# Optimization experiments

Measured on AMD Instinct MI355X. Metric: run time of the kernel, lower is better.

The kernel has to match this reference:

```python
import jax, jax.numpy as jnp
import numpy as np

D_MODEL = 1024
HEAD_SIZE = 64

def setup_inputs() -> dict:
    key = jax.random.key(0)
    ks = jax.random.split(key, 7)
    s = 1.0 / np.sqrt(D_MODEL)
    x = jax.random.normal(ks[0], (4, 4096, D_MODEL), dtype=jnp.float32)
    Wq = jax.random.uniform(ks[1], (D_MODEL, HEAD_SIZE), jnp.float32, -s, s)
    bq = jax.random.uniform(ks[2], (HEAD_SIZE,), jnp.float32, -s, s)
    Wk = jax.random.uniform(ks[3], (D_MODEL, HEAD_SIZE), jnp.float32, -s, s)
    bk = jax.random.uniform(ks[4], (HEAD_SIZE,), jnp.float32, -s, s)
    Wv = jax.random.uniform(ks[5], (D_MODEL, HEAD_SIZE), jnp.float32, -s, s)
    bv = jax.random.uniform(ks[6], (HEAD_SIZE,), jnp.float32, -s, s)
    return {"x": x, "Wq": Wq, "bq": bq, "Wk": Wk, "bk": bk, "Wv": Wv, "bv": bv}

def reference(x, Wq, bq, Wk, bk, Wv, bv):
    # x: [B, S, D]; projections to [B, S, H]
    Q = jnp.einsum('bsd,dh->bsh', x, Wq) + bq
    K = jnp.einsum('bsd,dh->bsh', x, Wk) + bk
    V = jnp.einsum('bsd,dh->bsh', x, Wv) + bv
    scores = jnp.einsum('bqh,bkh->bqk', Q, K) / jnp.sqrt(jnp.float32(HEAD_SIZE))
    attn = jax.nn.softmax(scores, axis=-1)  # [B, S, S]
    return jnp.einsum('bqk,bkh->bqh', attn, V)
```

## Files before the change

kernel.cpp:

```cpp
#include <hip/hip_runtime.h>
#include <hip/hip_bf16.h>


#define S_LEN 4096
#define D_MODEL 1024

typedef __attribute__((ext_vector_type(8))) short bf16x8;
typedef __attribute__((ext_vector_type(4))) float f32x4;
typedef __attribute__((ext_vector_type(16))) float f32x16;

__device__ inline short f2bf(float f) {
    union { float f; unsigned u; } v;
    v.f = f;
    unsigned r = v.u + 0x7fffu + ((v.u >> 16) & 1u);
    return (short)(r >> 16);
}

__device__ inline unsigned cvt_pk(float lo, float hi) {
    unsigned r;
    asm("v_cvt_pk_bf16_f32 %0, %1, %2" : "=v"(r) : "v"(lo), "v"(hi));
    return r;
}

__device__ inline void pl32swap(unsigned& a, unsigned& b) {
    asm("v_permlane32_swap_b32 %0, %1" : "+v"(a), "+v"(b));
}

__device__ inline f32x16 fzero16() {
    f32x16 z;
#pragma unroll
    for (int i = 0; i < 16; ++i) z[i] = 0.f;
    return z;
}

__device__ inline void gload_lds16(const void* g, void* l) {
    __builtin_amdgcn_global_load_lds((const __attribute__((address_space(1))) void*)g,
                                     (__attribute__((address_space(3))) void*)l, 16, 0, 0);
}

__global__ void prep_w(const float* __restrict__ Wq, const float* __restrict__ Wk,
                       const float* __restrict__ Wv, short* __restrict__ WtF) {
    int idx = blockIdx.x * 256 + threadIdx.x;
    int j = idx & 7;
    int lane = (idx >> 3) & 63;
    int f = idx >> 9;
    int ntg = f % 12;
    int kb = f / 12;
    int k = (kb >> 1) * 64 + (kb & 1) * 32 + (lane >> 4) * 8 + j;
    int c = ntg * 16 + (lane & 15);
    const float* W = (c < 64) ? Wq : (c < 128 ? Wk : Wv);
    WtF[idx] = f2bf(W[k * 64 + (c & 63)]);
}

__launch_bounds__(256)
__global__ void proj_kernel(const float* __restrict__ x, const short* __restrict__ WtF,
                            const float* __restrict__ bq, const float* __restrict__ bk,
                            const float* __restrict__ bv,
                            short* __restrict__ Qb, short* __restrict__ Kb,
                            short* __restrict__ Vt) {
    __shared__ short vsm[64][40];
    const float CEXP = 0.18033688011112042f;
    int w = threadIdx.x >> 6;
    int lane = threadIdx.x & 63;
    int g = lane >> 4, ln = lane & 15;
    int rt = w >> 1, nh = w & 1;
    int rowbase = blockIdx.x * 32;

    f32x4 acc[6];
#pragma unroll
    for (int i = 0; i < 6; ++i) acc[i] = (f32x4){0.f, 0.f, 0.f, 0.f};

    const float* xw = x + (size_t)(rowbase + rt * 16 + ln) * D_MODEL + g * 8;

    auto loadF = [&](bf16x8* F, int t) {
#pragma unroll
        for (int kk = 0; kk < 2; ++kk)
#pragma unroll
            for (int nt = 0; nt < 6; ++nt)
                F[kk * 6 + nt] = *(const bf16x8*)(WtF
                    + ((((t * 2 + kk) * 12 + nh * 6 + nt) << 9) + lane * 8));
    };

    auto computeF = [&](const bf16x8* F, const f32x4& X0, const f32x4& X1,
                        const f32x4& X2, const f32x4& X3) {
        union { bf16x8 v; unsigned u[4]; } A;
        A.u[0] = cvt_pk(X0[0], X0[1]);
        A.u[1] = cvt_pk(X0[2], X0[3]);
        A.u[2] = cvt_pk(X1[0], X1[1]);
        A.u[3] = cvt_pk(X1[2], X1[3]);
#pragma unroll
        for (int nt = 0; nt < 6; ++nt)
            acc[nt] = __builtin_amdgcn_mfma_f32_16x16x32_bf16(A.v, F[nt], acc[nt], 0, 0, 0);
        A.u[0] = cvt_pk(X2[0], X2[1]);
        A.u[1] = cvt_pk(X2[2], X2[3]);
        A.u[2] = cvt_pk(X3[0], X3[1]);
        A.u[3] = cvt_pk(X3[2], X3[3]);
#pragma unroll
        for (int nt = 0; nt < 6; ++nt)
            acc[nt] = __builtin_amdgcn_mfma_f32_16x16x32_bf16(A.v, F[6 + nt], acc[nt], 0, 0, 0);
    };

    bf16x8 Fa[12], Fb[12];
    loadF(Fa, 0);
    f32x4 XA0 = *(const f32x4*)(xw);
    f32x4 XA1 = *(const f32x4*)(xw + 4);
    f32x4 XA2 = *(const f32x4*)(xw + 32);
    f32x4 XA3 = *(const f32x4*)(xw + 36);
    f32x4 XB0 = *(const f32x4*)(xw + 64);
    f32x4 XB1 = *(const f32x4*)(xw + 68);
    f32x4 XB2 = *(const f32x4*)(xw + 96);
    f32x4 XB3 = *(const f32x4*)(xw + 100);

#pragma unroll 1
    for (int t = 0; t < 16; t += 2) {
        loadF(Fb, t + 1 > 15 ? 15 : t + 1);
        computeF(Fa, XA0, XA1, XA2, XA3);
        {
            int nx = t + 2 > 15 ? 15 : t + 2;
            const float* xn = xw + nx * 64;
            XA0 = *(const f32x4*)(xn);
            XA1 = *(const f32x4*)(xn + 4);
            XA2 = *(const f32x4*)(xn + 32);
            XA3 = *(const f32x4*)(xn + 36);
        }
        loadF(Fa, t + 2 > 15 ? 15 : t + 2);
        computeF(Fb, XB0, XB1, XB2, XB3);
        {
            int nx = t + 3 > 15 ? 15 : t + 3;
            const float* xn = xw + nx * 64;
            XB0 = *(const f32x4*)(xn);
            XB1 = *(const f32x4*)(xn + 4);
            XB2 = *(const f32x4*)(xn + 32);
            XB3 = *(const f32x4*)(xn + 36);
        }
    }

#pragma unroll
    for (int nt = 0; nt < 6; ++nt) {
        int c = nh * 96 + nt * 16 + ln;
        int proj = c >> 6;
        int h = c & 63;
        float bias = (proj == 0 ? bq : (proj == 1 ? bk : bv))[h];
#pragma unroll
        for (int r = 0; r < 4; ++r) {
            int srow = rowbase + rt * 16 + g * 4 + r;
            float v = acc[nt][r] + bias;
            if (proj == 0) v *= CEXP;
            short hv = f2bf(v);
            if (proj == 0) {
                Qb[(size_t)srow * 64 + h] = hv;
            } else if (proj == 1) {
                Kb[(size_t)srow * 64 + h] = hv;
            } else {
                vsm[h][rt * 16 + g * 4 + r] = hv;
            }
        }
    }
    __syncthreads();
    {
        int t = threadIdx.x;
        int h = t >> 2, c = t & 3;
        bf16x8 val = *(const bf16x8*)&vsm[h][c * 8];
        int bb = rowbase >> 12;
        int sg = (rowbase & 4095) + c * 8;
        *(bf16x8*)(Vt + ((size_t)(bb * 64 + h) << 12) + sg) = val;
    }
}

__launch_bounds__(512)
__global__ void attn_kernel(const short* __restrict__ Qb, const short* __restrict__ Kb,
                            const short* __restrict__ Vt, float* __restrict__ out) {
    __shared__ __align__(16) char smraw[131072];
    __shared__ float lsm[256];
    int lane = threadIdx.x & 63;
    int w = threadIdx.x >> 6;
    int l31 = lane & 31, hi = lane >> 5;
    int sp = w >> 1, qt = w & 1;

    int bid = blockIdx.x;
    int sb = (bid & 7) * 32 + (bid >> 3);
    int b = sb >> 6, qs = sb & 63;
    size_t qrow0 = ((size_t)b << 12) + (size_t)qs * 64;

    char* base = smraw + sp * 32768;
    char* kbuf = base;
    char* vbuf = base + 16384;

    const char* KB = (const char*)(Kb + (((size_t)b << 12) + sp * 1024) * 64);
    const char* VB = (const char*)Vt + (((size_t)b * 64) << 13) + (size_t)sp * 2048;

    auto stageT = [&](int buf, int t) {
        if (qt == 0) {
            char* dst = kbuf + buf * 8192;
#pragma unroll
            for (int i = 0; i < 8; ++i) {
                int od = i * 1024 + lane * 16;
                int row = od >> 7, colb = od & 127;
                const char* src = KB + (size_t)(t * 64 + row) * 128 + (colb ^ ((row & 7) << 4));
                gload_lds16(src, dst + i * 1024);
            }
        } else {
            char* dst = vbuf + buf * 8192;
#pragma unroll
            for (int i = 0; i < 8; ++i) {
                int od = i * 1024 + lane * 16;
                int row = od >> 7, colb = od & 127;
                const char* src = VB + (size_t)row * 8192 + t * 128 + (colb ^ ((row & 7) << 4));
                gload_lds16(src, dst + i * 1024);
            }
        }
    };

    bf16x8 qf[4];
    {
        const short* qp = Qb + (qrow0 + qt * 32 + l31) * 64 + hi * 8;
#pragma unroll
        for (int ks = 0; ks < 4; ++ks) qf[ks] = *(const bf16x8*)(qp + ks * 16);
    }

    f32x16 oacc0 = fzero16(), oacc1 = fzero16();
    float lacc[16];
#pragma unroll
    for (int r = 0; r < 16; ++r) lacc[r] = 0.f;

    int swz = (l31 & 7) << 4;
    stageT(0, 0);

#pragma unroll 1
    for (int t = 0; t < 16; ++t) {
        asm volatile("s_waitcnt vmcnt(0)" ::: "memory");
        __builtin_amdgcn_s_barrier();
        __builtin_amdgcn_sched_barrier(0);
        if (t < 15) stageT((t + 1) & 1, t + 1);

        const char* kc = kbuf + (t & 1) * 8192;
        const char* vc = vbuf + (t & 1) * 8192;

        bf16x8 kf[8];
#pragma unroll
        for (int kt = 0; kt < 2; ++kt)
#pragma unroll
            for (int ks = 0; ks < 4; ++ks)
                kf[kt * 4 + ks] = *(const bf16x8*)(kc + (kt * 32 + l31) * 128
                                                  + ((ks * 32 + hi * 16) ^ swz));
        f32x16 s0 = fzero16(), s1 = fzero16();
#pragma unroll
        for (int ks = 0; ks < 4; ++ks) {
            s0 = __builtin_amdgcn_mfma_f32_32x32x16_bf16(kf[ks], qf[ks], s0, 0, 0, 0);
            s1 = __builtin_amdgcn_mfma_f32_32x32x16_bf16(kf[4 + ks], qf[ks], s1, 0, 0, 0);
        }

        bf16x8 vf[8];
#pragma unroll
        for (int ht = 0; ht < 2; ++ht)
#pragma unroll
            for (int kk = 0; kk < 4; ++kk)
                vf[ht * 4 + kk] = *(const bf16x8*)(vc + (ht * 32 + l31) * 128
                                                   + ((kk * 32 + hi * 16) ^ swz));

        float p0[16], p1[16];
#pragma unroll
        for (int r = 0; r < 16; ++r) p0[r] = exp2f(s0[r]);
#pragma unroll
        for (int r = 0; r < 16; ++r) p1[r] = exp2f(s1[r]);
#pragma unroll
        for (int r = 0; r < 16; ++r) lacc[r] += p0[r] + p1[r];

        union { unsigned u[4]; bf16x8 v; } t00, t01, t10, t11;
        {
            unsigned D[8];
#pragma unroll
            for (int dw = 0; dw < 8; ++dw) D[dw] = cvt_pk(p0[2 * dw], p0[2 * dw + 1]);
            pl32swap(D[0], D[2]); pl32swap(D[1], D[3]);
            pl32swap(D[4], D[6]); pl32swap(D[5], D[7]);
            t00.u[0] = D[0]; t00.u[1] = D[1]; t00.u[2] = D[2]; t00.u[3] = D[3];
            t01.u[0] = D[4]; t01.u[1] = D[5]; t01.u[2] = D[6]; t01.u[3] = D[7];
        }
        {
            unsigned D[8];
#pragma unroll
            for (int dw = 0; dw < 8; ++dw) D[dw] = cvt_pk(p1[2 * dw], p1[2 * dw + 1]);
            pl32swap(D[0], D[2]); pl32swap(D[1], D[3]);
            pl32swap(D[4], D[6]); pl32swap(D[5], D[7]);
            t10.u[0] = D[0]; t10.u[1] = D[1]; t10.u[2] = D[2]; t10.u[3] = D[3];
            t11.u[0] = D[4]; t11.u[1] = D[5]; t11.u[2] = D[6]; t11.u[3] = D[7];
        }

        oacc0 = __builtin_amdgcn_mfma_f32_32x32x16_bf16(vf[0], t00.v, oacc0, 0, 0, 0);
        oacc1 = __builtin_amdgcn_mfma_f32_32x32x16_bf16(vf[4], t00.v, oacc1, 0, 0, 0);
        oacc0 = __builtin_amdgcn_mfma_f32_32x32x16_bf16(vf[1], t01.v, oacc0, 0, 0, 0);
        oacc1 = __builtin_amdgcn_mfma_f32_32x32x16_bf16(vf[5], t01.v, oacc1, 0, 0, 0);
        oacc0 = __builtin_amdgcn_mfma_f32_32x32x16_bf16(vf[2], t10.v, oacc0, 0, 0, 0);
        oacc1 = __builtin_amdgcn_mfma_f32_32x32x16_bf16(vf[6], t10.v, oacc1, 0, 0, 0);
        oacc0 = __builtin_amdgcn_mfma_f32_32x32x16_bf16(vf[3], t11.v, oacc0, 0, 0, 0);
        oacc1 = __builtin_amdgcn_mfma_f32_32x32x16_bf16(vf[7], t11.v, oacc1, 0, 0, 0);
    }

    float lfin;
    {
        float lt[8];
#pragma unroll
        for (int r = 0; r < 8; ++r) lt[r] = lacc[r] + lacc[r + 8];
#pragma unroll
        for (int st = 4; st >= 1; st >>= 1)
#pragma unroll
            for (int r = 0; r < 4; ++r)
                if (r < st) lt[r] += lt[r + st];
        lfin = lt[0] + __shfl_xor(lt[0], 32);
    }

    __syncthreads();
    float* osm = (float*)smraw;
    {
        float* ow = osm + (size_t)(w * 32 + l31) * 68;
#pragma unroll
        for (int r = 0; r < 16; ++r) {
            int h = (r & 3) + 8 * (r >> 2) + 4 * hi;
            ow[h] = oacc0[r];
            ow[32 + h] = oacc1[r];
        }
        if (hi == 0) lsm[w * 32 + l31] = lfin;
    }
    __syncthreads();
    {
        int tq = threadIdx.x >> 3, hb = (threadIdx.x & 7) * 8;
        int qt2 = tq >> 5, ql = tq & 31;
        f32x4 oa = (f32x4){0.f, 0.f, 0.f, 0.f}, ob = (f32x4){0.f, 0.f, 0.f, 0.f};
        float lsum = 0.f;
#pragma unroll
        for (int sp2 = 0; sp2 < 4; ++sp2) {
            int w2 = sp2 * 2 + qt2;
            lsum += lsm[w2 * 32 + ql];
            const float* src = osm + (size_t)(w2 * 32 + ql) * 68 + hb;
            f32x4 x0 = *(const f32x4*)src;
            f32x4 x1 = *(const f32x4*)(src + 4);
#pragma unroll
            for (int j = 0; j < 4; ++j) { oa[j] += x0[j]; ob[j] += x1[j]; }
        }
        float inv = 1.f / lsum;
        f32x4 r0, r1;
#pragma unroll
        for (int j = 0; j < 4; ++j) { r0[j] = oa[j] * inv; r1[j] = ob[j] * inv; }
        float* op = out + (qrow0 + tq) * 64 + hb;
        *(f32x4*)op = r0;
        *(f32x4*)(op + 4) = r1;
    }
}

extern "C" void kernel_launch(void* const* d_in, const int* in_sizes, int n_in,
                              void* d_out, int out_size, void* d_ws, size_t ws_size,
                              hipStream_t stream) {
    const float* x  = (const float*)d_in[0];
    const float* Wq = (const float*)d_in[1];
    const float* bq = (const float*)d_in[2];
    const float* Wk = (const float*)d_in[3];
    const float* bk = (const float*)d_in[4];
    const float* Wv = (const float*)d_in[5];
    const float* bv = (const float*)d_in[6];

    short* ws = (short*)d_ws;
    short* WtF = ws;
    short* Qb = WtF + 192 * 1024;
    short* Kb = Qb + 16384 * 64;
    short* Vt = Kb + 16384 * 64;

    prep_w<<<768, 256, 0, stream>>>(Wq, Wk, Wv, WtF);
    proj_kernel<<<512, 256, 0, stream>>>(x, WtF, bq, bk, bv, Qb, Kb, Vt);
    attn_kernel<<<256, 512, 0, stream>>>(Qb, Kb, Vt, (float*)d_out);
}
```

Before: 71.67 us.

## Halve proj_kernel row tile to 16 rows and split columns across four waves

Each projection block now covers 16 rows instead of 32, and each of its four waves computes 3 of the 12 output column tiles for all 16 rows. The grid doubles to 1024 blocks, and a min-blocks launch bound is added to raise occupancy for the memory-bound read of x. The trade-off is that each weight fragment is reused over fewer rows, so weight loads per row double, and the V transpose writes shrink to 8-byte stores.

```diff
diff --git a/kernel.cpp b/kernel.cpp
--- a/kernel.cpp
+++ b/kernel.cpp
@@ -52,33 +52,32 @@
     WtF[idx] = f2bf(W[k * 64 + (c & 63)]);
 }
 
-__launch_bounds__(256)
+__launch_bounds__(256, 5)
 __global__ void proj_kernel(const float* __restrict__ x, const short* __restrict__ WtF,
                             const float* __restrict__ bq, const float* __restrict__ bk,
                             const float* __restrict__ bv,
                             short* __restrict__ Qb, short* __restrict__ Kb,
                             short* __restrict__ Vt) {
-    __shared__ short vsm[64][40];
+    __shared__ short vsm[64][20];
     const float CEXP = 0.18033688011112042f;
     int w = threadIdx.x >> 6;
     int lane = threadIdx.x & 63;
     int g = lane >> 4, ln = lane & 15;
-    int rt = w >> 1, nh = w & 1;
-    int rowbase = blockIdx.x * 32;
-
-    f32x4 acc[6];
-#pragma unroll
-    for (int i = 0; i < 6; ++i) acc[i] = (f32x4){0.f, 0.f, 0.f, 0.f};
-
-    const float* xw = x + (size_t)(rowbase + rt * 16 + ln) * D_MODEL + g * 8;
+    int rowbase = blockIdx.x * 16;
+
+    f32x4 acc[3];
+#pragma unroll
+    for (int i = 0; i < 3; ++i) acc[i] = (f32x4){0.f, 0.f, 0.f, 0.f};
+
+    const float* xw = x + (size_t)(rowbase + ln) * D_MODEL + g * 8;
 
     auto loadF = [&](bf16x8* F, int t) {
 #pragma unroll
         for (int kk = 0; kk < 2; ++kk)
 #pragma unroll
-            for (int nt = 0; nt < 6; ++nt)
-                F[kk * 6 + nt] = *(const bf16x8*)(WtF
-                    + ((((t * 2 + kk) * 12 + nh * 6 + nt) << 9) + lane * 8));
+            for (int j = 0; j < 3; ++j)
+                F[kk * 3 + j] = *(const bf16x8*)(WtF
+                    + ((((t * 2 + kk) * 12 + w * 3 + j) << 9) + lane * 8));
     };
 
     auto computeF = [&](const bf16x8* F, const f32x4& X0, const f32x4& X1,
@@ -89,18 +88,18 @@
         A.u[2] = cvt_pk(X1[0], X1[1]);
         A.u[3] = cvt_pk(X1[2], X1[3]);
 #pragma unroll
-        for (int nt = 0; nt < 6; ++nt)
-            acc[nt] = __builtin_amdgcn_mfma_f32_16x16x32_bf16(A.v, F[nt], acc[nt], 0, 0, 0);
+        for (int j = 0; j < 3; ++j)
+            acc[j] = __builtin_amdgcn_mfma_f32_16x16x32_bf16(A.v, F[j], acc[j], 0, 0, 0);
         A.u[0] = cvt_pk(X2[0], X2[1]);
         A.u[1] = cvt_pk(X2[2], X2[3]);
         A.u[2] = cvt_pk(X3[0], X3[1]);
         A.u[3] = cvt_pk(X3[2], X3[3]);
 #pragma unroll
-        for (int nt = 0; nt < 6; ++nt)
-            acc[nt] = __builtin_amdgcn_mfma_f32_16x16x32_bf16(A.v, F[6 + nt], acc[nt], 0, 0, 0);
+        for (int j = 0; j < 3; ++j)
+            acc[j] = __builtin_amdgcn_mfma_f32_16x16x32_bf16(A.v, F[3 + j], acc[j], 0, 0, 0);
     };
 
-    bf16x8 Fa[12], Fb[12];
+    bf16x8 Fa[6], Fb[6];
     loadF(Fa, 0);
     f32x4 XA0 = *(const f32x4*)(xw);
     f32x4 XA1 = *(const f32x4*)(xw + 4);
@@ -136,15 +135,16 @@
     }
 
 #pragma unroll
-    for (int nt = 0; nt < 6; ++nt) {
-        int c = nh * 96 + nt * 16 + ln;
-        int proj = c >> 6;
+    for (int j = 0; j < 3; ++j) {
+        int ntg = w * 3 + j;
+        int c = ntg * 16 + ln;
+        int proj = ntg >> 2;
         int h = c & 63;
         float bias = (proj == 0 ? bq : (proj == 1 ? bk : bv))[h];
 #pragma unroll
         for (int r = 0; r < 4; ++r) {
-            int srow = rowbase + rt * 16 + g * 4 + r;
-            float v = acc[nt][r] + bias;
+            int srow = rowbase + g * 4 + r;
+            float v = acc[j][r] + bias;
             if (proj == 0) v *= CEXP;
             short hv = f2bf(v);
             if (proj == 0) {
@@ -152,18 +152,18 @@
             } else if (proj == 1) {
                 Kb[(size_t)srow * 64 + h] = hv;
             } else {
-                vsm[h][rt * 16 + g * 4 + r] = hv;
+                vsm[h][g * 4 + r] = hv;
             }
         }
     }
     __syncthreads();
     {
         int t = threadIdx.x;
-        int h = t >> 2, c = t & 3;
-        bf16x8 val = *(const bf16x8*)&vsm[h][c * 8];
+        int h = t >> 2, c4 = t & 3;
+        uint2 val = *(const uint2*)(&vsm[h][c4 * 4]);
         int bb = rowbase >> 12;
-        int sg = (rowbase & 4095) + c * 8;
-        *(bf16x8*)(Vt + ((size_t)(bb * 64 + h) << 12) + sg) = val;
+        int sg = (rowbase & 4095) + c4 * 4;
+        *(uint2*)(Vt + (((size_t)(bb * 64 + h)) << 12) + sg) = val;
     }
 }
 
@@ -365,6 +365,6 @@
     short* Vt = Kb + 16384 * 64;
 
     prep_w<<<768, 256, 0, stream>>>(Wq, Wk, Wv, WtF);
-    proj_kernel<<<512, 256, 0, stream>>>(x, WtF, bq, bk, bv, Qb, Kb, Vt);
+    proj_kernel<<<1024, 256, 0, stream>>>(x, WtF, bq, bk, bv, Qb, Kb, Vt);
     attn_kernel<<<256, 512, 0, stream>>>(Qb, Kb, Vt, (float*)d_out);
 }
```

Measured after the change: 85.03 us. +18.6%, slower.
